# Kernel optimization log

Measured on AMD Instinct MI355X. Metric: run time of the kernel, lower is better.

The kernel has to match this reference:

```python
import jax, jax.numpy as jnp
import numpy as np

D = 256          # config.entity_dim
DQ = 256         # query feature dim
G = 512          # number of neighbor groups (len(num_neighbors))
PER = 128
N = G * PER      # total candidate entities
CH = [256, 512, 512, 256]  # TCN channel list [D, 2D, 2D, D]
K = 3            # TCN kernel size
HID = 512        # policy net hidden dim


def _p(key, shape):
    return jax.random.normal(key, shape, dtype=jnp.float32) * 0.02


def setup_inputs() -> dict:
    key = jax.random.key(0)
    ks = jax.random.split(key, 32)
    inp = {}
    inp["NEs"] = jax.random.normal(ks[0], (N, D), dtype=jnp.float32)
    inp["nodes"] = jax.random.normal(ks[1], (G, D), dtype=jnp.float32)
    inp["query"] = jax.random.normal(ks[2], (G, DQ), dtype=jnp.float32)
    inp["num_neighbors"] = jnp.full((G,), PER, dtype=jnp.int32)
    inp["action_index"] = jax.random.randint(ks[3], (G,), 0, PER, dtype=jnp.int32)
    # action encoder (linear + relu)
    inp["Wa"] = _p(ks[4], (D, D))
    inp["ba"] = jnp.zeros((D,), jnp.float32)
    # TCN: 4 dilated causal conv levels, 1x1 downsample where channels change
    cin, i = D, 5
    for l, cout in enumerate(CH):
        inp[f"Wc{l}"] = _p(ks[i], (cout, cin, K)); i += 1
        inp[f"bc{l}"] = jnp.zeros((cout,), jnp.float32)
        if cout != cin:
            inp[f"Wd{l}"] = _p(ks[i], (cout, cin)); i += 1
        cin = cout
    # policy net MLP over [state_HS_per_candidate ; hat]
    inp["Wp1"] = _p(ks[i], (DQ + 2 * D + D, HID))
    inp["bp1"] = jnp.zeros((HID,), jnp.float32)
    inp["Wp2"] = _p(ks[i + 1], (HID, 1))
    inp["bp2"] = jnp.zeros((1,), jnp.float32)
    return inp


def _causal_conv(x, w, b, dil):
    # x: [1, C_in, L], w: [C_out, C_in, K] -> causal (left-padded) dilated conv
    k = w.shape[-1]
    y = jax.lax.conv_general_dilated(
        x, w, window_strides=(1,), padding=[((k - 1) * dil, 0)],
        rhs_dilation=(dil,), dimension_numbers=("NCH", "OIH", "NCH"))
    return y + b[None, :, None]


def _tcn(x, params):
    for (w, b, wd), dil in zip(params, (1, 2, 4, 8)):
        y = jax.nn.relu(_causal_conv(x, w, b, dil))
        res = x if wd is None else jnp.einsum("oi,bil->bol", wd, x)
        x = jax.nn.relu(y + res)
    return x


def reference(NEs, nodes, query, num_neighbors, action_index, Wa, ba,
              Wc0, bc0, Wc1, bc1, Wd1, Wc2, bc2, Wc3, bc3, Wd3,
              Wp1, bp1, Wp2, bp2):
    counts = np.asarray(num_neighbors)            # static ragged segment sizes
    g = counts.shape[0]
    seg = jnp.asarray(np.repeat(np.arange(g), counts))
    offsets = np.concatenate([[0], np.cumsum(counts)[:-1]])
    act = np.asarray(action_index)

    hats = jax.nn.relu(NEs @ Wa + ba)                         # [N, D]
    # _Max per group = column-wise max over each ragged segment
    HAts = jax.ops.segment_max(hats, seg, num_segments=g)     # [G, D]
    # chosen-action row per group (last group contributes no hat/node in the loop)
    hats_sel = hats[jnp.asarray(offsets[: g - 1] + act[: g - 1])]  # [G-1, D]

    # state_seq rows: (node_i, HAt_i, hat_i) for i < G-1, then nodes[-1]
    body = jnp.stack([nodes[: g - 1], HAts[: g - 1], hats_sel], axis=1)
    body = body.reshape(3 * (g - 1), -1)
    state_seq = jnp.concatenate([body, nodes[-1:]], axis=0)   # [L, D], L = 3(G-1)+1

    x = state_seq.T[None]                                     # [1, D, L]
    x = _tcn(x, [(Wc0, bc0, None), (Wc1, bc1, Wd1), (Wc2, bc2, None), (Wc3, bc3, Wd3)])
    hs = x[0].T[np.arange(g) * 3]                             # gather node positions -> [G, D]

    state_HS = jnp.concatenate([query, hs, HAts], axis=1)     # [G, DQ + 2D]
    rep = jnp.repeat(state_HS, jnp.asarray(counts), axis=0)   # [N, DQ + 2D]
    h = jax.nn.relu(jnp.concatenate([rep, hats], axis=1) @ Wp1 + bp1)
    Qsa = h @ Wp2 + bp2                                       # [N, 1]
    return Qsa
```

## Files before the change

kernel.cpp:

```cpp
#include <hip/hip_runtime.h>
#include <hip/hip_bf16.h>

#define D 256
#define G 512
#define PER 128
#define NROW (G*PER)
#define LSEQ 1534
#define LP 1536
#define HID 512

typedef __hip_bfloat16 bf16;
typedef __attribute__((ext_vector_type(8))) short bf16x8;
typedef __attribute__((ext_vector_type(4))) float f32x4;


__global__ __launch_bounds__(256) void k_prep(
    const float* __restrict__ Wa, bf16* __restrict__ WAhi, bf16* __restrict__ WAlo,
    const float* __restrict__ Wp1, bf16* __restrict__ WBt,
    bf16* __restrict__ WB1hi, bf16* __restrict__ WB1lo) {
  const int b = blockIdx.x, tid = threadIdx.x;
  if (b < 256) {
    int id = b * 256 + tid;
    int k = id >> 8, n = id & 255;
    float v = Wa[(size_t)k * D + n];
    bf16 h = __float2bfloat16(v);
    bf16 l = __float2bfloat16(v - __bfloat162float(h));
    int dst = (n >> 7) * 32768
            + (((((n >> 4) & 7) * 8 + (k >> 5)) * 64 + ((k >> 3) & 3) * 16 + (n & 15)) * 8)
            + (k & 7);
    WAhi[dst] = h;
    WAlo[dst] = l;
  } else if (b < 768) {
    int id = (b - 256) * 256 + tid;
    int k = id >> 9, n = id & 511;
    float v = Wp1[(size_t)(768 + k) * HID + n];
    int dst = (n >> 7) * 32768
            + (((((n >> 4) & 7) * 8 + (k >> 5)) * 64 + ((k >> 3) & 3) * 16 + (n & 15)) * 8)
            + (k & 7);
    WBt[dst] = __float2bfloat16(v);
  } else {
    int id = (b - 768) * 256 + tid;
    int k = id >> 9, n = id & 511;
    float v = Wp1[(size_t)k * HID + n];
    bf16 h = __float2bfloat16(v);
    bf16 l = __float2bfloat16(v - __bfloat162float(h));
    int kc = k >> 8, kr = k & 255;
    int nc = n >> 7, nr = n & 127;
    int dst = (nc*3 + kc) * 32768
            + ((((nr >> 4) * 8 + (kr >> 5)) * 64 + ((kr >> 3) & 3) * 16 + (nr & 15)) * 8)
            + (kr & 7);
    WB1hi[dst] = h;
    WB1lo[dst] = l;
  }
}

__global__ __launch_bounds__(512) void k_hats_mfma(
    const float* __restrict__ NEs, const bf16* __restrict__ WAhi,
    const bf16* __restrict__ WAlo, const float* __restrict__ ba,
    bf16* __restrict__ hats, float* __restrict__ HAts) {
  __shared__ __align__(16) unsigned short bs[36864];
  __shared__ float wsmax[8][128];

  const int tid = threadIdx.x;
  const int wave = tid >> 6, lane = tid & 63;
  const int ln = lane & 15, quad = lane >> 4;
  const int row0 = blockIdx.x * 128;
  const int g = blockIdx.x;

  bf16x8 afH[8], afL[8];
  {
    const float4* ap = (const float4*)(NEs + (size_t)(row0 + wave*16 + ln) * D);
    #pragma unroll
    for (int kt = 0; kt < 8; ++kt) {
      float4 x0 = ap[kt*8 + quad*2];
      float4 x1 = ap[kt*8 + quad*2 + 1];
      float xv[8] = {x0.x, x0.y, x0.z, x0.w, x1.x, x1.y, x1.z, x1.w};
      bf16x8 hv, lv;
      #pragma unroll
      for (int e = 0; e < 8; ++e) {
        bf16 h = __float2bfloat16(xv[e]);
        bf16 l = __float2bfloat16(xv[e] - __bfloat162float(h));
        hv[e] = *(short*)&h;
        lv[e] = *(short*)&l;
      }
      afH[kt] = hv;
      afL[kt] = lv;
    }
  }

  float* bsf = (float*)bs;

  for (int chunk = 0; chunk < 2; ++chunk) {
    f32x4 acc[8];
    #pragma unroll
    for (int nt = 0; nt < 8; ++nt) acc[nt] = (f32x4){0.f, 0.f, 0.f, 0.f};

    __syncthreads();
    {
      const uint4* src = (const uint4*)(WAhi + (size_t)chunk * 32768);
      uint4* dst = (uint4*)bs;
      #pragma unroll
      for (int r = 0; r < 8; ++r) dst[r*512 + tid] = src[r*512 + tid];
    }
    __syncthreads();
    #pragma unroll
    for (int nt = 0; nt < 8; ++nt)
      #pragma unroll
      for (int kt = 0; kt < 8; ++kt) {
        const bf16x8 bfr = *(const bf16x8*)&bs[((nt*8 + kt)*64 + lane)*8];
        acc[nt] = __builtin_amdgcn_mfma_f32_16x16x32_bf16(afH[kt], bfr, acc[nt], 0, 0, 0);
        acc[nt] = __builtin_amdgcn_mfma_f32_16x16x32_bf16(afL[kt], bfr, acc[nt], 0, 0, 0);
      }

    __syncthreads();
    {
      const uint4* src = (const uint4*)(WAlo + (size_t)chunk * 32768);
      uint4* dst = (uint4*)bs;
      #pragma unroll
      for (int r = 0; r < 8; ++r) dst[r*512 + tid] = src[r*512 + tid];
    }
    __syncthreads();
    #pragma unroll
    for (int nt = 0; nt < 8; ++nt)
      #pragma unroll
      for (int kt = 0; kt < 8; ++kt) {
        const bf16x8 bfr = *(const bf16x8*)&bs[((nt*8 + kt)*64 + lane)*8];
        acc[nt] = __builtin_amdgcn_mfma_f32_16x16x32_bf16(afH[kt], bfr, acc[nt], 0, 0, 0);
      }

    __syncthreads();
    #pragma unroll
    for (int nt = 0; nt < 8; ++nt) {
      const float bv = ba[chunk*128 + nt*16 + ln];
      float m = 0.f;
      #pragma unroll
      for (int reg = 0; reg < 4; ++reg) {
        float h = acc[nt][reg] + bv;
        h = h > 0.f ? h : 0.f;
        bsf[(wave*16 + quad*4 + reg)*140 + nt*16 + ln] = h;
        m = fmaxf(m, h);
      }
      m = fmaxf(m, __shfl_xor(m, 16, 64));
      m = fmaxf(m, __shfl_xor(m, 32, 64));
      if (quad == 0) wsmax[wave][nt*16 + ln] = m;
    }
    __syncthreads();
    {
      const int row = tid >> 2, q4 = tid & 3;
      const float* rp = &bsf[row*140 + q4*32];
      bf16* gp = hats + (size_t)(row0 + row) * D + chunk*128 + q4*32;
      #pragma unroll
      for (int s = 0; s < 4; ++s) {
        float4 v0 = *(const float4*)&rp[s*8];
        float4 v1 = *(const float4*)&rp[s*8 + 4];
        float vv[8] = {v0.x, v0.y, v0.z, v0.w, v1.x, v1.y, v1.z, v1.w};
        bf16x8 pk;
        #pragma unroll
        for (int e = 0; e < 8; ++e) {
          bf16 b = __float2bfloat16(vv[e]);
          pk[e] = *(short*)&b;
        }
        *(bf16x8*)(gp + s*8) = pk;
      }
    }
    if (tid < 128) {
      float m = wsmax[0][tid];
      #pragma unroll
      for (int w = 1; w < 8; ++w) m = fmaxf(m, wsmax[w][tid]);
      HAts[(size_t)g*D + chunk*128 + tid] = m;
    }
  }
}

__global__ void k_sprep(const float* __restrict__ query,
                        const float* __restrict__ HAts,
                        const float* __restrict__ xfin,
                        bf16* __restrict__ Shi, bf16* __restrict__ Slo) {
  int m = blockIdx.x * 256 + threadIdx.x;
  int g = blockIdx.y;
  float v;
  if (m < 256)      v = query[(size_t)g*D + m];
  else if (m < 512) v = xfin[(size_t)(m - 256)*LP + 3*g];
  else              v = HAts[(size_t)g*D + (m - 512)];
  bf16 h = __float2bfloat16(v);
  bf16 l = __float2bfloat16(v - __bfloat162float(h));
  Shi[(size_t)g*768 + m] = h;
  Slo[(size_t)g*768 + m] = l;
}

__global__ __launch_bounds__(256) void k_gterm_mfma(
    const bf16* __restrict__ Shi, const bf16* __restrict__ Slo,
    const bf16* __restrict__ WB1hi, const bf16* __restrict__ WB1lo,
    const float* __restrict__ bp1, float* __restrict__ Gterm) {
  __shared__ __align__(16) unsigned short bs[32768];

  const int tid = threadIdx.x;
  const int wave = tid >> 6, lane = tid & 63;
  const int ln = lane & 15, quad = lane >> 4;
  const int nc = blockIdx.x;
  const int row0 = blockIdx.y * 64;

  f32x4 acc[8];
  #pragma unroll
  for (int nt = 0; nt < 8; ++nt) acc[nt] = (f32x4){0.f, 0.f, 0.f, 0.f};

  const uint4* ahp = (const uint4*)(Shi + (size_t)(row0 + wave*16 + ln) * 768);
  const uint4* alp = (const uint4*)(Slo + (size_t)(row0 + wave*16 + ln) * 768);

  for (int kc = 0; kc < 3; ++kc) {
    bf16x8 afH[8], afL[8];
    #pragma unroll
    for (int kt = 0; kt < 8; ++kt) {
      uint4 th = ahp[kc*32 + kt*4 + quad];
      uint4 tl = alp[kc*32 + kt*4 + quad];
      afH[kt] = *(const bf16x8*)&th;
      afL[kt] = *(const bf16x8*)&tl;
    }

    __syncthreads();
    {
      const uint4* src = (const uint4*)(WB1hi + (size_t)(nc*3 + kc) * 32768);
      uint4* dst = (uint4*)bs;
      #pragma unroll
      for (int r = 0; r < 16; ++r) dst[r*256 + tid] = src[r*256 + tid];
    }
    __syncthreads();
    #pragma unroll
    for (int nt = 0; nt < 8; ++nt)
      #pragma unroll
      for (int kt = 0; kt < 8; ++kt) {
        const bf16x8 bfr = *(const bf16x8*)&bs[((nt*8 + kt)*64 + lane)*8];
        acc[nt] = __builtin_amdgcn_mfma_f32_16x16x32_bf16(afH[kt], bfr, acc[nt], 0, 0, 0);
        acc[nt] = __builtin_amdgcn_mfma_f32_16x16x32_bf16(afL[kt], bfr, acc[nt], 0, 0, 0);
      }

    __syncthreads();
    {
      const uint4* src = (const uint4*)(WB1lo + (size_t)(nc*3 + kc) * 32768);
      uint4* dst = (uint4*)bs;
      #pragma unroll
      for (int r = 0; r < 16; ++r) dst[r*256 + tid] = src[r*256 + tid];
    }
    __syncthreads();
    #pragma unroll
    for (int nt = 0; nt < 8; ++nt)
      #pragma unroll
      for (int kt = 0; kt < 8; ++kt) {
        const bf16x8 bfr = *(const bf16x8*)&bs[((nt*8 + kt)*64 + lane)*8];
        acc[nt] = __builtin_amdgcn_mfma_f32_16x16x32_bf16(afH[kt], bfr, acc[nt], 0, 0, 0);
      }
  }

  #pragma unroll
  for (int nt = 0; nt < 8; ++nt) {
    const int col = nc*128 + nt*16 + ln;
    const float bv = bp1[col];
    #pragma unroll
    for (int reg = 0; reg < 4; ++reg)
      Gterm[(size_t)(row0 + wave*16 + quad*4 + reg) * HID + col] = acc[nt][reg] + bv;
  }
}

__global__ void k_build_x0(const float* __restrict__ nodes,
                           const float* __restrict__ HAts,
                           const bf16* __restrict__ hats,
                           const int* __restrict__ act,
                           float* __restrict__ x0) {
  int t = blockIdx.x * 256 + threadIdx.x;
  int c = blockIdx.y;
  if (t >= LSEQ) return;
  float v;
  if (t == LSEQ - 1) {
    v = nodes[(size_t)(G-1)*D + c];
  } else {
    int r = t / 3, m = t - 3*r;
    if (m == 0)      v = nodes[(size_t)r*D + c];
    else if (m == 1) v = HAts[(size_t)r*D + c];
    else             v = __bfloat162float(hats[(size_t)(r*PER + act[r])*D + c]);
  }
  x0[(size_t)c*LP + t] = v;
}

template<int DIL, int CPB, bool HASWD>
__global__ __launch_bounds__(256) void k_tcn4(
    const float* __restrict__ xin,
    const float* __restrict__ W,
    const float* __restrict__ Wd,
    float* __restrict__ ybuf,
    float* __restrict__ rbuf,
    int Cin) {
  __shared__ __align__(16) float xs[32][80];
  __shared__ __align__(16) float wst[3][32][68];
  __shared__ __align__(16) float wds[HASWD ? 32 : 1][HASWD ? 68 : 4];

  const int tid = threadIdx.x;
  const int tt = tid & 15;
  const int cc = tid >> 4;
  const int t0 = blockIdx.x * 64;
  const int o0 = blockIdx.y * 64;
  const int Cout = gridDim.y << 6;

  float acc[4][4], res[4][4];
  #pragma unroll
  for (int it = 0; it < 4; ++it)
    #pragma unroll
    for (int ic = 0; ic < 4; ++ic) { acc[it][ic] = 0.f; res[it][ic] = 0.f; }

  for (int c = 0; c < CPB; ++c) {
    const int i0 = (blockIdx.z * CPB + c) * 32;
    __syncthreads();
    for (int idx = tid; idx < 32*20; idx += 256) {
      int r = idx / 20, j4 = idx - r*20;
      int tp = t0 - 16 + j4*4;
      float4 v;
      if (tp >= 0) v = *(const float4*)&xin[(size_t)(i0 + r)*LP + tp];
      else         v = make_float4(0.f, 0.f, 0.f, 0.f);
      *(float4*)&xs[r][j4*4] = v;
    }
    for (int idx = tid; idx < 64*32; idx += 256) {
      int o = idx >> 5, i = idx & 31;
      const float* wp = &W[((size_t)(o0 + o)*Cin + i0 + i)*3];
      wst[0][i][o] = wp[0];
      wst[1][i][o] = wp[1];
      wst[2][i][o] = wp[2];
      if constexpr (HASWD) wds[i][o] = Wd[(size_t)(o0 + o)*Cin + i0 + i];
    }
    __syncthreads();

    const int base = 16 + tt*4;
    #pragma unroll 2
    for (int i = 0; i < 32; ++i) {
      float4 xv0, xv1, xv2;
      if constexpr (DIL == 1) {
        float4 A = *(const float4*)&xs[i][base - 4];
        float4 B = *(const float4*)&xs[i][base];
        xv0 = make_float4(A.z, A.w, B.x, B.y);
        xv1 = make_float4(A.w, B.x, B.y, B.z);
        xv2 = B;
      } else if constexpr (DIL == 2) {
        float4 A = *(const float4*)&xs[i][base - 4];
        float4 B = *(const float4*)&xs[i][base];
        xv0 = A;
        xv1 = make_float4(A.z, A.w, B.x, B.y);
        xv2 = B;
      } else {
        xv0 = *(const float4*)&xs[i][base - 2*DIL];
        xv1 = *(const float4*)&xs[i][base - DIL];
        xv2 = *(const float4*)&xs[i][base];
      }
      float4 w0 = *(const float4*)&wst[0][i][cc*4];
      float4 w1 = *(const float4*)&wst[1][i][cc*4];
      float4 w2 = *(const float4*)&wst[2][i][cc*4];
      #pragma unroll
      for (int it = 0; it < 4; ++it) {
        float x0 = ((const float*)&xv0)[it];
        float x1 = ((const float*)&xv1)[it];
        float x2 = ((const float*)&xv2)[it];
        #pragma unroll
        for (int ic = 0; ic < 4; ++ic) {
          float a = acc[it][ic];
          a = fmaf(x0, ((const float*)&w0)[ic], a);
          a = fmaf(x1, ((const float*)&w1)[ic], a);
          a = fmaf(x2, ((const float*)&w2)[ic], a);
          acc[it][ic] = a;
        }
      }
      if constexpr (HASWD) {
        float4 wd4 = *(const float4*)&wds[i][cc*4];
        #pragma unroll
        for (int it = 0; it < 4; ++it) {
          float x2 = ((const float*)&xv2)[it];
          #pragma unroll
          for (int ic = 0; ic < 4; ++ic)
            res[it][ic] = fmaf(x2, ((const float*)&wd4)[ic], res[it][ic]);
        }
      }
    }
  }

  const int t = t0 + tt*4;
  #pragma unroll
  for (int ic = 0; ic < 4; ++ic) {
    const int ch = o0 + cc*4 + ic;
    const size_t off = ((size_t)blockIdx.z * Cout + ch) * LP + t;
    float4 v = make_float4(acc[0][ic], acc[1][ic], acc[2][ic], acc[3][ic]);
    *(float4*)&ybuf[off] = v;
    if constexpr (HASWD) {
      float4 rv = make_float4(res[0][ic], res[1][ic], res[2][ic], res[3][ic]);
      *(float4*)&rbuf[off] = rv;
    }
  }
}

template<int NZ, bool HASWD>
__global__ __launch_bounds__(384) void k_tcn_red(
    const float* __restrict__ ybuf, const float* __restrict__ rbuf,
    const float* __restrict__ xin, const float* __restrict__ b,
    float* __restrict__ xout) {
  const int ch = blockIdx.x;
  const int Cout = gridDim.x;
  const int t = threadIdx.x * 4;
  const size_t stride = (size_t)Cout * LP;
  const size_t base = (size_t)ch * LP + t;

  float4 y = *(const float4*)&ybuf[base];
  #pragma unroll
  for (int z = 1; z < NZ; ++z) {
    float4 u = *(const float4*)&ybuf[base + z*stride];
    y.x += u.x; y.y += u.y; y.z += u.z; y.w += u.w;
  }
  const float bv = b[ch];
  y.x = fmaxf(y.x + bv, 0.f); y.y = fmaxf(y.y + bv, 0.f);
  y.z = fmaxf(y.z + bv, 0.f); y.w = fmaxf(y.w + bv, 0.f);

  float4 r;
  if constexpr (HASWD) {
    r = *(const float4*)&rbuf[base];
    #pragma unroll
    for (int z = 1; z < NZ; ++z) {
      float4 u = *(const float4*)&rbuf[base + z*stride];
      r.x += u.x; r.y += u.y; r.z += u.z; r.w += u.w;
    }
  } else {
    r = *(const float4*)&xin[base];
  }
  float4 v;
  v.x = fmaxf(y.x + r.x, 0.f); v.y = fmaxf(y.y + r.y, 0.f);
  v.z = fmaxf(y.z + r.z, 0.f); v.w = fmaxf(y.w + r.w, 0.f);
  *(float4*)&xout[base] = v;
}

__global__ __launch_bounds__(512) void k_final_mfma(
    const bf16* __restrict__ hats, const bf16* __restrict__ WBt,
    const float* __restrict__ Gterm, const float* __restrict__ Wp2,
    const float* __restrict__ bp2, float* __restrict__ out) {
  __shared__ __align__(16) unsigned short bs[32768];
  __shared__ float gs[512];
  __shared__ float w2s[512];

  const int tid = threadIdx.x;
  const int wave = tid >> 6, lane = tid & 63;
  const int ln = lane & 15, quad = lane >> 4;
  const int row0 = blockIdx.x * 128;
  const int g = blockIdx.x;

  gs[tid]  = Gterm[(size_t)g*HID + tid];
  w2s[tid] = Wp2[tid];

  bf16x8 afrag[8];
  {
    const uint4* ap = (const uint4*)(hats + (size_t)(row0 + wave*16 + ln) * D);
    #pragma unroll
    for (int kt = 0; kt < 8; ++kt) {
      uint4 t = ap[kt*4 + quad];
      afrag[kt] = *(const bf16x8*)&t;
    }
  }

  float osum[4] = {0.f, 0.f, 0.f, 0.f};

  for (int chunk = 0; chunk < 4; ++chunk) {
    __syncthreads();
    const uint4* src = (const uint4*)(WBt + (size_t)chunk * 32768);
    uint4* dst = (uint4*)bs;
    #pragma unroll
    for (int r = 0; r < 8; ++r) dst[r*512 + tid] = src[r*512 + tid];
    __syncthreads();

    #pragma unroll
    for (int nt = 0; nt < 8; ++nt) {
      f32x4 acc = {0.f, 0.f, 0.f, 0.f};
      #pragma unroll
      for (int kt = 0; kt < 8; ++kt) {
        const bf16x8 bfr = *(const bf16x8*)&bs[((nt*8 + kt)*64 + lane)*8];
        acc = __builtin_amdgcn_mfma_f32_16x16x32_bf16(afrag[kt], bfr, acc, 0, 0, 0);
      }
      int n = chunk*128 + nt*16 + ln;
      float gv = gs[n], wv = w2s[n];
      #pragma unroll
      for (int reg = 0; reg < 4; ++reg) {
        float h = acc[reg] + gv;
        h = h > 0.f ? h : 0.f;
        osum[reg] = fmaf(h, wv, osum[reg]);
      }
    }
  }

  #pragma unroll
  for (int reg = 0; reg < 4; ++reg) {
    float v = osum[reg];
    v += __shfl_xor(v, 1, 64);
    v += __shfl_xor(v, 2, 64);
    v += __shfl_xor(v, 4, 64);
    v += __shfl_xor(v, 8, 64);
    osum[reg] = v;
  }
  if (ln == 0) {
    float b2 = bp2[0];
    #pragma unroll
    for (int reg = 0; reg < 4; ++reg)
      out[row0 + wave*16 + quad*4 + reg] = osum[reg] + b2;
  }
}

extern "C" void kernel_launch(void* const* d_in, const int* in_sizes, int n_in,
                              void* d_out, int out_size, void* d_ws, size_t ws_size,
                              hipStream_t stream) {
  (void)in_sizes; (void)n_in; (void)out_size; (void)ws_size;
  const float* NEs   = (const float*)d_in[0];
  const float* nodes = (const float*)d_in[1];
  const float* query = (const float*)d_in[2];
  const int*   act   = (const int*)d_in[4];
  const float* Wa    = (const float*)d_in[5];
  const float* ba    = (const float*)d_in[6];
  const float* Wc0   = (const float*)d_in[7];
  const float* bc0   = (const float*)d_in[8];
  const float* Wc1   = (const float*)d_in[9];
  const float* bc1   = (const float*)d_in[10];
  const float* Wd1   = (const float*)d_in[11];
  const float* Wc2   = (const float*)d_in[12];
  const float* bc2   = (const float*)d_in[13];
  const float* Wc3   = (const float*)d_in[14];
  const float* bc3   = (const float*)d_in[15];
  const float* Wd3   = (const float*)d_in[16];
  const float* Wp1   = (const float*)d_in[17];
  const float* bp1   = (const float*)d_in[18];
  const float* Wp2   = (const float*)d_in[19];
  const float* bp2   = (const float*)d_in[20];
  float* out = (float*)d_out;

  char* ws = (char*)d_ws;
  bf16*  hats  = (bf16*)ws;  ws += (size_t)NROW * D * sizeof(bf16);
  float* HAts  = (float*)ws; ws += (size_t)G * D * sizeof(float);
  float* xa    = (float*)ws; ws += (size_t)512 * LP * sizeof(float);
  float* xb    = (float*)ws; ws += (size_t)512 * LP * sizeof(float);
  float* Gterm = (float*)ws; ws += (size_t)G * HID * sizeof(float);
  bf16*  WBt   = (bf16*)ws;  ws += (size_t)D * HID * sizeof(bf16);
  bf16*  WAhi  = (bf16*)ws;  ws += (size_t)D * D * sizeof(bf16);
  bf16*  WAlo  = (bf16*)ws;  ws += (size_t)D * D * sizeof(bf16);
  bf16*  WB1hi = (bf16*)ws;  ws += (size_t)768 * HID * sizeof(bf16);
  bf16*  WB1lo = (bf16*)ws;  ws += (size_t)768 * HID * sizeof(bf16);
  bf16*  Shi   = (bf16*)ws;  ws += (size_t)G * 768 * sizeof(bf16);
  bf16*  Slo   = (bf16*)ws;  ws += (size_t)G * 768 * sizeof(bf16);
  float* P0 = (float*)ws; ws += (size_t)2048 * LP * sizeof(float);
  float* P1 = (float*)ws; ws += (size_t)2048 * LP * sizeof(float);

  k_prep<<<2304, 256, 0, stream>>>(Wa, WAhi, WAlo, Wp1, WBt, WB1hi, WB1lo);
  k_hats_mfma<<<G, 512, 0, stream>>>(NEs, WAhi, WAlo, ba, hats, HAts);
  k_build_x0<<<dim3(6, 256), 256, 0, stream>>>(nodes, HAts, hats, act, xa);

  k_tcn4<1, 1, false><<<dim3(24, 4, 8), 256, 0, stream>>>(xa, Wc0, nullptr, P0, nullptr, 256);
  k_tcn_red<8, false><<<256, 384, 0, stream>>>(P0, nullptr, xa, bc0, xb);
  k_tcn4<2, 2, true ><<<dim3(24, 8, 4), 256, 0, stream>>>(xb, Wc1, Wd1, P0, P1, 256);
  k_tcn_red<4, true ><<<512, 384, 0, stream>>>(P0, P1, xb, bc1, xa);
  k_tcn4<4, 4, false><<<dim3(24, 8, 4), 256, 0, stream>>>(xa, Wc2, nullptr, P0, nullptr, 512);
  k_tcn_red<4, false><<<512, 384, 0, stream>>>(P0, nullptr, xa, bc2, xb);
  k_tcn4<8, 2, true ><<<dim3(24, 4, 8), 256, 0, stream>>>(xb, Wc3, Wd3, P0, P1, 512);
  k_tcn_red<8, true ><<<256, 384, 0, stream>>>(P0, P1, xb, bc3, xa);

  k_sprep<<<dim3(3, G), 256, 0, stream>>>(query, HAts, xa, Shi, Slo);
  k_gterm_mfma<<<dim3(4, 8), 256, 0, stream>>>(Shi, Slo, WB1hi, WB1lo, bp1, Gterm);
  k_final_mfma<<<G, 512, 0, stream>>>(hats, WBt, Gterm, Wp2, bp2, out);
}
```

Baseline: 355.5 us.

## Give each wave two row tiles in hats and final MFMA kernels

Both MFMA kernels (k_hats_mfma and k_final_mfma) drop from 512 to 256 threads per block. Each wave now computes two 16-row tiles instead of one, so every B fragment read from LDS feeds two MFMAs. This is meant to halve LDS read traffic per MFMA and shrink the k_hats shared buffer. The costs are higher VGPR pressure from the doubled A fragments and accumulators, fewer waves per CU to hide latency, and a serialized two-pass epilogue in the hats kernel.

Result: no change. 354.4 us (-0.3%).

```diff
diff --git a/kernel.cpp b/kernel.cpp
--- a/kernel.cpp
+++ b/kernel.cpp
@@ -54,11 +54,11 @@
   }
 }
 
-__global__ __launch_bounds__(512) void k_hats_mfma(
+__global__ __launch_bounds__(256, 2) void k_hats_mfma(
     const float* __restrict__ NEs, const bf16* __restrict__ WAhi,
     const bf16* __restrict__ WAlo, const float* __restrict__ ba,
     bf16* __restrict__ hats, float* __restrict__ HAts) {
-  __shared__ __align__(16) unsigned short bs[36864];
+  __shared__ __align__(16) unsigned short bs[32768];
   __shared__ float wsmax[8][128];
 
   const int tid = threadIdx.x;
@@ -67,9 +67,10 @@
   const int row0 = blockIdx.x * 128;
   const int g = blockIdx.x;
 
-  bf16x8 afH[8], afL[8];
-  {
-    const float4* ap = (const float4*)(NEs + (size_t)(row0 + wave*16 + ln) * D);
+  bf16x8 afH[2][8], afL[2][8];
+  #pragma unroll
+  for (int t = 0; t < 2; ++t) {
+    const float4* ap = (const float4*)(NEs + (size_t)(row0 + (t*4 + wave)*16 + ln) * D);
     #pragma unroll
     for (int kt = 0; kt < 8; ++kt) {
       float4 x0 = ap[kt*8 + quad*2];
@@ -83,24 +84,26 @@
         hv[e] = *(short*)&h;
         lv[e] = *(short*)&l;
       }
-      afH[kt] = hv;
-      afL[kt] = lv;
+      afH[t][kt] = hv;
+      afL[t][kt] = lv;
     }
   }
 
   float* bsf = (float*)bs;
 
   for (int chunk = 0; chunk < 2; ++chunk) {
-    f32x4 acc[8];
-    #pragma unroll
-    for (int nt = 0; nt < 8; ++nt) acc[nt] = (f32x4){0.f, 0.f, 0.f, 0.f};
+    f32x4 acc[2][8];
+    #pragma unroll
+    for (int t = 0; t < 2; ++t)
+      #pragma unroll
+      for (int nt = 0; nt < 8; ++nt) acc[t][nt] = (f32x4){0.f, 0.f, 0.f, 0.f};
 
     __syncthreads();
     {
       const uint4* src = (const uint4*)(WAhi + (size_t)chunk * 32768);
       uint4* dst = (uint4*)bs;
       #pragma unroll
-      for (int r = 0; r < 8; ++r) dst[r*512 + tid] = src[r*512 + tid];
+      for (int r = 0; r < 16; ++r) dst[r*256 + tid] = src[r*256 + tid];
     }
     __syncthreads();
     #pragma unroll
@@ -108,8 +111,10 @@
       #pragma unroll
       for (int kt = 0; kt < 8; ++kt) {
         const bf16x8 bfr = *(const bf16x8*)&bs[((nt*8 + kt)*64 + lane)*8];
-        acc[nt] = __builtin_amdgcn_mfma_f32_16x16x32_bf16(afH[kt], bfr, acc[nt], 0, 0, 0);
-        acc[nt] = __builtin_amdgcn_mfma_f32_16x16x32_bf16(afL[kt], bfr, acc[nt], 0, 0, 0);
+        acc[0][nt] = __builtin_amdgcn_mfma_f32_16x16x32_bf16(afH[0][kt], bfr, acc[0][nt], 0, 0, 0);
+        acc[1][nt] = __builtin_amdgcn_mfma_f32_16x16x32_bf16(afH[1][kt], bfr, acc[1][nt], 0, 0, 0);
+        acc[0][nt] = __builtin_amdgcn_mfma_f32_16x16x32_bf16(afL[0][kt], bfr, acc[0][nt], 0, 0, 0);
+        acc[1][nt] = __builtin_amdgcn_mfma_f32_16x16x32_bf16(afL[1][kt], bfr, acc[1][nt], 0, 0, 0);
       }
 
     __syncthreads();
@@ -117,7 +122,7 @@
       const uint4* src = (const uint4*)(WAlo + (size_t)chunk * 32768);
       uint4* dst = (uint4*)bs;
       #pragma unroll
-      for (int r = 0; r < 8; ++r) dst[r*512 + tid] = src[r*512 + tid];
+      for (int r = 0; r < 16; ++r) dst[r*256 + tid] = src[r*256 + tid];
     }
     __syncthreads();
     #pragma unroll
@@ -125,42 +130,46 @@
       #pragma unroll
       for (int kt = 0; kt < 8; ++kt) {
         const bf16x8 bfr = *(const bf16x8*)&bs[((nt*8 + kt)*64 + lane)*8];
-        acc[nt] = __builtin_amdgcn_mfma_f32_16x16x32_bf16(afH[kt], bfr, acc[nt], 0, 0, 0);
-      }
-
-    __syncthreads();
-    #pragma unroll
-    for (int nt = 0; nt < 8; ++nt) {
-      const float bv = ba[chunk*128 + nt*16 + ln];
-      float m = 0.f;
-      #pragma unroll
-      for (int reg = 0; reg < 4; ++reg) {
-        float h = acc[nt][reg] + bv;
-        h = h > 0.f ? h : 0.f;
-        bsf[(wave*16 + quad*4 + reg)*140 + nt*16 + ln] = h;
-        m = fmaxf(m, h);
-      }
-      m = fmaxf(m, __shfl_xor(m, 16, 64));
-      m = fmaxf(m, __shfl_xor(m, 32, 64));
-      if (quad == 0) wsmax[wave][nt*16 + ln] = m;
-    }
-    __syncthreads();
-    {
-      const int row = tid >> 2, q4 = tid & 3;
-      const float* rp = &bsf[row*140 + q4*32];
-      bf16* gp = hats + (size_t)(row0 + row) * D + chunk*128 + q4*32;
-      #pragma unroll
-      for (int s = 0; s < 4; ++s) {
-        float4 v0 = *(const float4*)&rp[s*8];
-        float4 v1 = *(const float4*)&rp[s*8 + 4];
-        float vv[8] = {v0.x, v0.y, v0.z, v0.w, v1.x, v1.y, v1.z, v1.w};
-        bf16x8 pk;
+        acc[0][nt] = __builtin_amdgcn_mfma_f32_16x16x32_bf16(afH[0][kt], bfr, acc[0][nt], 0, 0, 0);
+        acc[1][nt] = __builtin_amdgcn_mfma_f32_16x16x32_bf16(afH[1][kt], bfr, acc[1][nt], 0, 0, 0);
+      }
+
+    #pragma unroll
+    for (int t = 0; t < 2; ++t) {
+      __syncthreads();
+      #pragma unroll
+      for (int nt = 0; nt < 8; ++nt) {
+        const float bv = ba[chunk*128 + nt*16 + ln];
+        float m = 0.f;
         #pragma unroll
-        for (int e = 0; e < 8; ++e) {
-          bf16 b = __float2bfloat16(vv[e]);
-          pk[e] = *(short*)&b;
+        for (int reg = 0; reg < 4; ++reg) {
+          float h = acc[t][nt][reg] + bv;
+          h = h > 0.f ? h : 0.f;
+          bsf[(wave*16 + quad*4 + reg)*140 + nt*16 + ln] = h;
+          m = fmaxf(m, h);
         }
-        *(bf16x8*)(gp + s*8) = pk;
+        m = fmaxf(m, __shfl_xor(m, 16, 64));
+        m = fmaxf(m, __shfl_xor(m, 32, 64));
+        if (quad == 0) wsmax[t*4 + wave][nt*16 + ln] = m;
+      }
+      __syncthreads();
+      {
+        const int row = tid >> 2, q4 = tid & 3;
+        const float* rp = &bsf[row*140 + q4*32];
+        bf16* gp = hats + (size_t)(row0 + t*64 + row) * D + chunk*128 + q4*32;
+        #pragma unroll
+        for (int s = 0; s < 4; ++s) {
+          float4 v0 = *(const float4*)&rp[s*8];
+          float4 v1 = *(const float4*)&rp[s*8 + 4];
+          float vv[8] = {v0.x, v0.y, v0.z, v0.w, v1.x, v1.y, v1.z, v1.w};
+          bf16x8 pk;
+          #pragma unroll
+          for (int e = 0; e < 8; ++e) {
+            bf16 b = __float2bfloat16(vv[e]);
+            pk[e] = *(short*)&b;
+          }
+          *(bf16x8*)(gp + s*8) = pk;
+        }
       }
     }
     if (tid < 128) {
@@ -430,7 +439,7 @@
   *(float4*)&xout[base] = v;
 }
 
-__global__ __launch_bounds__(512) void k_final_mfma(
+__global__ __launch_bounds__(256, 2) void k_final_mfma(
     const bf16* __restrict__ hats, const bf16* __restrict__ WBt,
     const float* __restrict__ Gterm, const float* __restrict__ Wp2,
     const float* __restrict__ bp2, float* __restrict__ out) {
@@ -444,62 +453,74 @@
   const int row0 = blockIdx.x * 128;
   const int g = blockIdx.x;
 
-  gs[tid]  = Gterm[(size_t)g*HID + tid];
-  w2s[tid] = Wp2[tid];
-
-  bf16x8 afrag[8];
-  {
-    const uint4* ap = (const uint4*)(hats + (size_t)(row0 + wave*16 + ln) * D);
+  gs[tid]        = Gterm[(size_t)g*HID + tid];
+  gs[tid + 256]  = Gterm[(size_t)g*HID + tid + 256];
+  w2s[tid]       = Wp2[tid];
+  w2s[tid + 256] = Wp2[tid + 256];
+
+  bf16x8 afrag[2][8];
+  #pragma unroll
+  for (int t = 0; t < 2; ++t) {
+    const uint4* ap = (const uint4*)(hats + (size_t)(row0 + (t*4 + wave)*16 + ln) * D);
     #pragma unroll
     for (int kt = 0; kt < 8; ++kt) {
-      uint4 t = ap[kt*4 + quad];
-      afrag[kt] = *(const bf16x8*)&t;
-    }
-  }
-
-  float osum[4] = {0.f, 0.f, 0.f, 0.f};
+      uint4 u = ap[kt*4 + quad];
+      afrag[t][kt] = *(const bf16x8*)&u;
+    }
+  }
+
+  float osum[2][4] = {{0.f,0.f,0.f,0.f},{0.f,0.f,0.f,0.f}};
 
   for (int chunk = 0; chunk < 4; ++chunk) {
     __syncthreads();
     const uint4* src = (const uint4*)(WBt + (size_t)chunk * 32768);
     uint4* dst = (uint4*)bs;
     #pragma unroll
-    for (int r = 0; r < 8; ++r) dst[r*512 + tid] = src[r*512 + tid];
+    for (int r = 0; r < 16; ++r) dst[r*256 + tid] = src[r*256 + tid];
     __syncthreads();
 
     #pragma unroll
     for (int nt = 0; nt < 8; ++nt) {
-      f32x4 acc = {0.f, 0.f, 0.f, 0.f};
+      f32x4 acc0 = {0.f, 0.f, 0.f, 0.f};
+      f32x4 acc1 = {0.f, 0.f, 0.f, 0.f};
       #pragma unroll
       for (int kt = 0; kt < 8; ++kt) {
         const bf16x8 bfr = *(const bf16x8*)&bs[((nt*8 + kt)*64 + lane)*8];
-        acc = __builtin_amdgcn_mfma_f32_16x16x32_bf16(afrag[kt], bfr, acc, 0, 0, 0);
+        acc0 = __builtin_amdgcn_mfma_f32_16x16x32_bf16(afrag[0][kt], bfr, acc0, 0, 0, 0);
+        acc1 = __builtin_amdgcn_mfma_f32_16x16x32_bf16(afrag[1][kt], bfr, acc1, 0, 0, 0);
       }
       int n = chunk*128 + nt*16 + ln;
       float gv = gs[n], wv = w2s[n];
       #pragma unroll
       for (int reg = 0; reg < 4; ++reg) {
-        float h = acc[reg] + gv;
-        h = h > 0.f ? h : 0.f;
-        osum[reg] = fmaf(h, wv, osum[reg]);
-      }
-    }
-  }
-
-  #pragma unroll
-  for (int reg = 0; reg < 4; ++reg) {
-    float v = osum[reg];
-    v += __shfl_xor(v, 1, 64);
-    v += __shfl_xor(v, 2, 64);
-    v += __shfl_xor(v, 4, 64);
-    v += __shfl_xor(v, 8, 64);
-    osum[reg] = v;
-  }
+        float h0 = acc0[reg] + gv;
+        h0 = h0 > 0.f ? h0 : 0.f;
+        osum[0][reg] = fmaf(h0, wv, osum[0][reg]);
+        float h1 = acc1[reg] + gv;
+        h1 = h1 > 0.f ? h1 : 0.f;
+        osum[1][reg] = fmaf(h1, wv, osum[1][reg]);
+      }
+    }
+  }
+
+  #pragma unroll
+  for (int t = 0; t < 2; ++t)
+    #pragma unroll
+    for (int reg = 0; reg < 4; ++reg) {
+      float v = osum[t][reg];
+      v += __shfl_xor(v, 1, 64);
+      v += __shfl_xor(v, 2, 64);
+      v += __shfl_xor(v, 4, 64);
+      v += __shfl_xor(v, 8, 64);
+      osum[t][reg] = v;
+    }
   if (ln == 0) {
     float b2 = bp2[0];
     #pragma unroll
-    for (int reg = 0; reg < 4; ++reg)
-      out[row0 + wave*16 + quad*4 + reg] = osum[reg] + b2;
+    for (int t = 0; t < 2; ++t)
+      #pragma unroll
+      for (int reg = 0; reg < 4; ++reg)
+        out[row0 + (t*4 + wave)*16 + quad*4 + reg] = osum[t][reg] + b2;
   }
 }
 
@@ -546,7 +567,7 @@
   float* P1 = (float*)ws; ws += (size_t)2048 * LP * sizeof(float);
 
   k_prep<<<2304, 256, 0, stream>>>(Wa, WAhi, WAlo, Wp1, WBt, WB1hi, WB1lo);
-  k_hats_mfma<<<G, 512, 0, stream>>>(NEs, WAhi, WAlo, ba, hats, HAts);
+  k_hats_mfma<<<G, 256, 0, stream>>>(NEs, WAhi, WAlo, ba, hats, HAts);
   k_build_x0<<<dim3(6, 256), 256, 0, stream>>>(nodes, HAts, hats, act, xa);
 
   k_tcn4<1, 1, false><<<dim3(24, 4, 8), 256, 0, stream>>>(xa, Wc0, nullptr, P0, nullptr, 256);
@@ -560,5 +581,5 @@
 
   k_sprep<<<dim3(3, G), 256, 0, stream>>>(query, HAts, xa, Shi, Slo);
   k_gterm_mfma<<<dim3(4, 8), 256, 0, stream>>>(Shi, Slo, WB1hi, WB1lo, bp1, Gterm);
-  k_final_mfma<<<G, 512, 0, stream>>>(hats, WBt, Gterm, Wp2, bp2, out);
-}
+  k_final_mfma<<<G, 256, 0, stream>>>(hats, WBt, Gterm, Wp2, bp2, out);
+}
```
